# Kernel tuning notes

Hardware: AMD Instinct MI355X
Metric: run time of the kernel (lower is better)

## Reference

```python
import jax, jax.numpy as jnp
import numpy as np

N = 400000      # total atoms across batch of molecules
E = 1600000     # directed edges (avg degree 4)
G = 4096        # number of graphs (molecules)
F_IN = 78       # atomic feature size
H = 128         # gnn hidden dims (gnn_0 = gnn_1 = 128)
FF0, FF1 = 256, 128


def _lin(k, fan_in, fan_out):
    return jax.random.normal(k, (fan_in, fan_out), jnp.float32) / np.sqrt(fan_in).astype(np.float32)


def setup_inputs() -> dict:
    key = jax.random.key(0)
    ks = jax.random.split(key, 10)
    x = jax.random.normal(ks[0], (N, F_IN), jnp.float32)
    edge_index = jax.random.randint(ks[1], (2, E), 0, N, dtype=jnp.int64)
    # sorted graph ids, guaranteed non-empty segments (empty segment -> -inf under max pool)
    batch = (jnp.arange(N, dtype=jnp.int64) * G) // N
    return {
        'x': x, 'edge_index': edge_index, 'batch': batch,
        'W0': _lin(ks[2], F_IN, H), 'b0': jnp.zeros((H,), jnp.float32),
        'W1': _lin(ks[3], H, H),    'b1': jnp.zeros((H,), jnp.float32),
        'Wf0': _lin(ks[4], H, FF0), 'bf0': jnp.zeros((FF0,), jnp.float32),
        'Wf1': _lin(ks[5], FF0, FF1), 'bf1': jnp.zeros((FF1,), jnp.float32),
    }


def _gcn_conv(h, W, b, src, dst, dinv):
    # GCNConv with add_self_loops=True, symmetric normalization.
    hw = h @ W                                     # [N, out]
    norm = dinv[src] * dinv[dst]                   # [E]
    msg = hw[src] * norm[:, None]                  # gather + scale
    agg = jax.ops.segment_sum(msg, dst, num_segments=h.shape[0])
    agg = agg + hw * (dinv * dinv)[:, None]        # self-loop contribution
    return agg + b


def reference(x, edge_index, batch, W0, b0, W1, b1, Wf0, bf0, Wf1, bf1):
    src, dst = edge_index[0], edge_index[1]
    # degree of A + I computed at target nodes (PyG gcn_norm uses col)
    deg = jax.ops.segment_sum(jnp.ones((E,), x.dtype), dst, num_segments=N) + 1.0
    dinv = jax.lax.rsqrt(deg)

    h = jax.nn.relu(_gcn_conv(x, W0, b0, src, dst, dinv))
    h = jax.nn.relu(_gcn_conv(h, W1, b1, src, dst, dinv))

    g = jax.ops.segment_max(h, batch, num_segments=G)   # global max pool [G, H]

    g = jax.nn.relu(g @ Wf0 + bf0)   # dropout is identity in eval
    g = jax.nn.relu(g @ Wf1 + bf1)
    return g
```

## Files before the change

kernel.cpp:

```cpp
#include <hip/hip_runtime.h>
#include <cstdint>
#include <cstddef>

#define NATOMS 400000
#define NEDGES 1600000
#define NGRAPH 4096
#define F_INN  78
#define HDIM   128
#define FF0D   256
#define FF1D   128

typedef __attribute__((ext_vector_type(8))) short short8;
typedef __attribute__((ext_vector_type(4))) short short4v;
typedef __attribute__((ext_vector_type(4))) float f32x4;
typedef __attribute__((ext_vector_type(2))) float f32x2;

static __device__ __forceinline__ short f2bf(float f) {
    unsigned u = __builtin_bit_cast(unsigned, f);
    unsigned r = (u + 0x7fffu + ((u >> 16) & 1u)) >> 16;
    return (short)r;
}
static __device__ __forceinline__ float bf2f(unsigned short u) {
    return __builtin_bit_cast(float, ((unsigned)u) << 16);
}

__global__ __launch_bounds__(256) void k_degi(const int* __restrict__ dst,
                                              int* __restrict__ deg,
                                              int* __restrict__ rank, int E) {
    int e = blockIdx.x * 256 + threadIdx.x;
    if (e < E) rank[e] = atomicAdd(&deg[dst[e]], 1);
}

__global__ __launch_bounds__(256) void k_scan1(int* __restrict__ data,
                                               int* __restrict__ blockSums,
                                               float* __restrict__ dinv, int n) {
    __shared__ int ts[256];
    const int base = blockIdx.x * 1024 + threadIdx.x * 4;
    int v[4];
    #pragma unroll
    for (int j = 0; j < 4; ++j) v[j] = (base + j < n) ? data[base + j] : 0;
    #pragma unroll
    for (int j = 0; j < 4; ++j)
        if (base + j < n) dinv[base + j] = rsqrtf((float)v[j] + 1.0f);
    const int tot = v[0] + v[1] + v[2] + v[3];
    ts[threadIdx.x] = tot;
    __syncthreads();
    #pragma unroll
    for (int off = 1; off < 256; off <<= 1) {
        int t = (threadIdx.x >= off) ? ts[threadIdx.x - off] : 0;
        __syncthreads();
        ts[threadIdx.x] += t;
        __syncthreads();
    }
    int run = ts[threadIdx.x] - tot;
    #pragma unroll
    for (int j = 0; j < 4; ++j) {
        if (base + j < n) data[base + j] = run;
        run += v[j];
    }
    if (threadIdx.x == 255) blockSums[blockIdx.x] = ts[255];
}

__global__ __launch_bounds__(512) void k_scan2(int* __restrict__ blockSums, int nb) {
    __shared__ int ts[512];
    int v = (threadIdx.x < nb) ? blockSums[threadIdx.x] : 0;
    ts[threadIdx.x] = v;
    __syncthreads();
    #pragma unroll
    for (int off = 1; off < 512; off <<= 1) {
        int t = (threadIdx.x >= off) ? ts[threadIdx.x - off] : 0;
        __syncthreads();
        ts[threadIdx.x] += t;
        __syncthreads();
    }
    if (threadIdx.x < nb) blockSums[threadIdx.x] = ts[threadIdx.x] - v;
}

__global__ __launch_bounds__(256) void k_scan3(int* __restrict__ data,
                                               const int* __restrict__ blockSums,
                                               int n, int total) {
    const int off = blockSums[blockIdx.x];
    const int base = blockIdx.x * 1024 + threadIdx.x * 4;
    #pragma unroll
    for (int j = 0; j < 4; ++j)
        if (base + j < n) data[base + j] += off;
    if (blockIdx.x == 0 && threadIdx.x == 0) data[n] = total;
}

__global__ __launch_bounds__(256) void k_fill(const int* __restrict__ src,
                                              const int* __restrict__ dst,
                                              const int* __restrict__ row_start,
                                              const int* __restrict__ rank,
                                              int2* __restrict__ csr_ev,
                                              const float* __restrict__ dinv, int E) {
    int e = blockIdx.x * 256 + threadIdx.x;
    if (e >= E) return;
    int d = dst[e];
    int s = src[e];
    int pos = row_start[d] + rank[e];
    float norm = dinv[s] * dinv[d];
    csr_ev[pos] = make_int2(s, __builtin_bit_cast(int, norm));
}

template<int KC, int KSRC>
__global__ __launch_bounds__(64) void k_packw(const float* __restrict__ W,
                                              short* __restrict__ wf) {
    int t = blockIdx.x * 64 + threadIdx.x;
    int f = t >> 6, lane = t & 63;
    int ct = f / KC, kc = f % KC;
    int n  = ct * 16 + (lane & 15);
    int k0 = kc * 32 + (lane >> 4) * 8;
    short8 o;
    #pragma unroll
    for (int j = 0; j < 8; ++j) {
        int k = k0 + j;
        float v = (k < KSRC) ? W[(size_t)k * 128 + n] : 0.f;
        o[j] = f2bf(v);
    }
    *(short8*)(wf + (size_t)t * 8) = o;
}

template<int KC, bool F32IN, int KSRC>
__global__ __launch_bounds__(256) void k_gemm_mfma(
    const void* __restrict__ inv, const short* __restrict__ wfrag,
    short* __restrict__ outp, int M)
{
    constexpr int NFRAG = 8 * KC;
    __shared__ short lds_w[NFRAG * 64 * 8];

    const int tid = threadIdx.x;
    #pragma unroll
    for (int it = 0; it < NFRAG * 64 / 256; ++it) {
        int t = it * 256 + tid;
        *(short8*)(lds_w + (size_t)t * 8) = *(const short8*)(wfrag + (size_t)t * 8);
    }
    __syncthreads();

    const int lane = tid & 63;
    const int m = lane & 15, q = lane >> 4;
    const int gw = blockIdx.x * 4 + (tid >> 6);
    const int NW = gridDim.x * 4;
    const int NTILE = M / 16;

    auto load_afr = [&](int tile, short8* afr) {
        const int rowa = tile * 16 + m;
        if constexpr (F32IN) {
            const float* xr = (const float*)inv + (size_t)rowa * KSRC;
            #pragma unroll
            for (int kc = 0; kc < KC; ++kc) {
                const int k0 = kc * 32 + q * 8;
                float v[8];
                #pragma unroll
                for (int j = 0; j < 8; ++j) v[j] = 0.f;
                if (k0 < KSRC) {
                    #pragma unroll
                    for (int p = 0; p < 4; ++p) {
                        int k = k0 + 2 * p;
                        if (k < KSRC) {
                            f32x2 t = *(const f32x2*)(xr + k);
                            v[2 * p] = t.x; v[2 * p + 1] = t.y;
                        }
                    }
                }
                short8 a;
                #pragma unroll
                for (int j = 0; j < 8; ++j) a[j] = f2bf(v[j]);
                afr[kc] = a;
            }
        } else {
            const short* xr = (const short*)inv + (size_t)rowa * KSRC;
            #pragma unroll
            for (int kc = 0; kc < KC; ++kc)
                afr[kc] = *(const short8*)(xr + kc * 32 + q * 8);
        }
    };

    short8 afr[KC], afrN[KC];
    load_afr(gw, afr);

    for (int t = gw; t < NTILE; t += NW) {
        const int tn = t + NW;
        if (tn < NTILE) load_afr(tn, afrN);

        f32x4 acc[8];
        #pragma unroll
        for (int ct = 0; ct < 8; ++ct) acc[ct] = (f32x4){0.f, 0.f, 0.f, 0.f};
        #pragma unroll
        for (int kc = 0; kc < KC; ++kc)
            #pragma unroll
            for (int ct = 0; ct < 8; ++ct) {
                const short8 wv = *(const short8*)(lds_w + ((size_t)((ct * KC + kc) * 64 + lane)) * 8);
                acc[ct] = __builtin_amdgcn_mfma_f32_16x16x32_bf16(wv, afr[kc], acc[ct], 0, 0, 0);
            }

        const size_t nodeoff = (size_t)(t * 16 + m) * 128;
        #pragma unroll
        for (int ct = 0; ct < 8; ++ct) {
            short4v o;
            o.x = f2bf(acc[ct][0]);
            o.y = f2bf(acc[ct][1]);
            o.z = f2bf(acc[ct][2]);
            o.w = f2bf(acc[ct][3]);
            *(short4v*)(outp + nodeoff + ct * 16 + q * 4) = o;
        }

        #pragma unroll
        for (int kc = 0; kc < KC; ++kc) afr[kc] = afrN[kc];
    }
}

__global__ __launch_bounds__(256) void k_gather_bf(
    const unsigned short* __restrict__ hw, unsigned short* __restrict__ agg,
    const int* __restrict__ row_start, const int2* __restrict__ csr_ev,
    const float* __restrict__ dinv, const float* __restrict__ bias, int Nn)
{
    const int n  = blockIdx.x * 16 + (threadIdx.x >> 4);
    const int c8 = (threadIdx.x & 15) * 8;
    const float dv = dinv[n];
    const float d2 = dv * dv;

    float acc[8];
    {
        const short8 sv = *(const short8*)(hw + (size_t)n * HDIM + c8);
        #pragma unroll
        for (int j = 0; j < 8; ++j)
            acc[j] = fmaf(bf2f((unsigned short)sv[j]), d2, bias[c8 + j]);
    }

    const int s0 = row_start[n], s1 = row_start[n + 1];
    int i = s0;
    for (; i + 3 < s1; i += 4) {
        const int2 e0 = csr_ev[i];
        const int2 e1 = csr_ev[i + 1];
        const int2 e2 = csr_ev[i + 2];
        const int2 e3 = csr_ev[i + 3];
        const short8 r0 = *(const short8*)(hw + (size_t)e0.x * HDIM + c8);
        const short8 r1 = *(const short8*)(hw + (size_t)e1.x * HDIM + c8);
        const short8 r2 = *(const short8*)(hw + (size_t)e2.x * HDIM + c8);
        const short8 r3 = *(const short8*)(hw + (size_t)e3.x * HDIM + c8);
        const float w0 = __builtin_bit_cast(float, e0.y);
        const float w1 = __builtin_bit_cast(float, e1.y);
        const float w2 = __builtin_bit_cast(float, e2.y);
        const float w3 = __builtin_bit_cast(float, e3.y);
        #pragma unroll
        for (int j = 0; j < 8; ++j) acc[j] = fmaf(bf2f((unsigned short)r0[j]), w0, acc[j]);
        #pragma unroll
        for (int j = 0; j < 8; ++j) acc[j] = fmaf(bf2f((unsigned short)r1[j]), w1, acc[j]);
        #pragma unroll
        for (int j = 0; j < 8; ++j) acc[j] = fmaf(bf2f((unsigned short)r2[j]), w2, acc[j]);
        #pragma unroll
        for (int j = 0; j < 8; ++j) acc[j] = fmaf(bf2f((unsigned short)r3[j]), w3, acc[j]);
    }
    for (; i < s1; ++i) {
        const int2 e0 = csr_ev[i];
        const short8 r0 = *(const short8*)(hw + (size_t)e0.x * HDIM + c8);
        const float w0 = __builtin_bit_cast(float, e0.y);
        #pragma unroll
        for (int j = 0; j < 8; ++j) acc[j] = fmaf(bf2f((unsigned short)r0[j]), w0, acc[j]);
    }

    short8 o;
    #pragma unroll
    for (int j = 0; j < 8; ++j) o[j] = f2bf(fmaxf(acc[j], 0.f));
    __builtin_nontemporal_store(o, (short8*)(agg + (size_t)n * HDIM + c8));
}

__global__ __launch_bounds__(256) void k_pool(
    const unsigned short* __restrict__ agg,
    const int* __restrict__ batch, float* __restrict__ out, int Nn)
{
    __shared__ int se[2];
    __shared__ float red[256];
    int g = blockIdx.x;
    if (threadIdx.x < 2) {
        int target = g + (int)threadIdx.x;
        int lo = 0, hi = Nn;
        while (lo < hi) {
            int mid = (lo + hi) >> 1;
            if (batch[mid] < target) lo = mid + 1; else hi = mid;
        }
        se[threadIdx.x] = lo;
    }
    __syncthreads();
    const int start = se[0], end = se[1];
    const int c = threadIdx.x & 127;
    const int half = threadIdx.x >> 7;
    float m = 0.f;
    for (int i = start + half; i < end; i += 2)
        m = fmaxf(m, bf2f(__builtin_nontemporal_load(agg + (size_t)i * HDIM + c)));
    red[threadIdx.x] = m;
    __syncthreads();
    if (half == 0)
        out[(size_t)g * HDIM + c] = fmaxf(red[threadIdx.x], red[threadIdx.x + 128]);
}

template<int K, int NC, bool OUT_RELU_BIAS>
__global__ __launch_bounds__(256) void k_gemm(
    const float* __restrict__ in, const float* __restrict__ W,
    const float* __restrict__ out_bias, float* __restrict__ out0, int M)
{
    constexpr int BK = 32;
    constexpr int TC = NC / 8;
    constexpr int TR = 256 / TC;
    constexpr int ROWS = TR * 8;
    constexpr int XST = ROWS + 4;

    __shared__ float xs[BK][XST];
    __shared__ float ws[BK][NC];

    const int tid = threadIdx.x;
    const int tc  = tid % TC;
    const int tr  = tid / TC;
    const int row0 = blockIdx.x * ROWS;

    float acc[8][8];
    #pragma unroll
    for (int i = 0; i < 8; ++i)
        #pragma unroll
        for (int j = 0; j < 8; ++j) acc[i][j] = 0.f;

    for (int k0 = 0; k0 < K; k0 += BK) {
        {
            constexpr int TASKS = BK * NC / 4;
            #pragma unroll
            for (int it = 0; it < TASKS / 256; ++it) {
                int t  = it * 256 + tid;
                int wk = t / (NC / 4);
                int wc = (t % (NC / 4)) * 4;
                *(float4*)(&ws[wk][wc]) = *(const float4*)(W + (size_t)(k0 + wk) * NC + wc);
            }
        }
        {
            constexpr int TASKS = ROWS * BK / 4;
            #pragma unroll
            for (int it = 0; it < TASKS / 256; ++it) {
                int t   = it * 256 + tid;
                int r   = t / (BK / 4);
                int kq  = (t % (BK / 4)) * 4;
                float4 x4 = *(const float4*)(in + (size_t)(row0 + r) * K + k0 + kq);
                xs[kq + 0][r] = x4.x; xs[kq + 1][r] = x4.y;
                xs[kq + 2][r] = x4.z; xs[kq + 3][r] = x4.w;
            }
        }
        __syncthreads();
        #pragma unroll 8
        for (int kk = 0; kk < BK; ++kk) {
            float a[8], b[8];
            #pragma unroll
            for (int i = 0; i < 8; ++i) a[i] = xs[kk][tr * 8 + i];
            #pragma unroll
            for (int j = 0; j < 8; ++j) b[j] = ws[kk][tc * 8 + j];
            #pragma unroll
            for (int i = 0; i < 8; ++i)
                #pragma unroll
                for (int j = 0; j < 8; ++j)
                    acc[i][j] = fmaf(a[i], b[j], acc[i][j]);
        }
        __syncthreads();
    }

    #pragma unroll
    for (int i = 0; i < 8; ++i) {
        const int row = row0 + tr * 8 + i;
        #pragma unroll
        for (int jq = 0; jq < 2; ++jq) {
            const int col = tc * 8 + jq * 4;
            float4 v;
            v.x = acc[i][jq * 4 + 0]; v.y = acc[i][jq * 4 + 1];
            v.z = acc[i][jq * 4 + 2]; v.w = acc[i][jq * 4 + 3];
            if constexpr (OUT_RELU_BIAS) {
                const float4 bb = *(const float4*)(out_bias + col);
                v.x = fmaxf(v.x + bb.x, 0.f); v.y = fmaxf(v.y + bb.y, 0.f);
                v.z = fmaxf(v.z + bb.z, 0.f); v.w = fmaxf(v.w + bb.w, 0.f);
            }
            *(float4*)(out0 + (size_t)row * NC + col) = v;
        }
    }
}

extern "C" void kernel_launch(void* const* d_in, const int* in_sizes, int n_in,
                              void* d_out, int out_size, void* d_ws, size_t ws_size,
                              hipStream_t stream) {
    const float* x    = (const float*)d_in[0];
    const int*   ei   = (const int*)d_in[1];
    const int*   batch= (const int*)d_in[2];
    const float* W0   = (const float*)d_in[3];
    const float* b0   = (const float*)d_in[4];
    const float* W1   = (const float*)d_in[5];
    const float* b1   = (const float*)d_in[6];
    const float* Wf0  = (const float*)d_in[7];
    const float* bf0  = (const float*)d_in[8];
    const float* Wf1  = (const float*)d_in[9];
    const float* bf1  = (const float*)d_in[10];
    float* out = (float*)d_out;

    const int* srcI = ei;
    const int* dstI = ei + NEDGES;

    constexpr int SCAN_NBLK = (NATOMS + 1023) / 1024;

    char* base = (char*)d_ws;
    unsigned short* hwA  = (unsigned short*)(base + 0);
    unsigned short* aggB = (unsigned short*)(base + 102400000);
    int*   rank      = (int*)(base + 102400000);
    float* dinv      = (float*)(base + 204800000);
    int*   row_start = (int*)(base + 206400000);
    int2*  csr_ev    = (int2*)(base + 208000064);
    int*   blockSums = (int*)(base + 220800064);
    float* pool      = (float*)(base + 220802112);
    float* ff0       = (float*)(base + 222899264);
    short* wf0       = (short*)(base + 227093568);
    short* wf1       = (short*)(base + 227118144);

    hipMemsetAsync(row_start, 0, (size_t)(NATOMS + 1) * sizeof(int), stream);
    k_degi<<<(NEDGES + 255) / 256, 256, 0, stream>>>(dstI, row_start, rank, NEDGES);
    k_scan1<<<SCAN_NBLK, 256, 0, stream>>>(row_start, blockSums, dinv, NATOMS);
    k_scan2<<<1, 512, 0, stream>>>(blockSums, SCAN_NBLK);
    k_scan3<<<SCAN_NBLK, 256, 0, stream>>>(row_start, blockSums, NATOMS, NEDGES);
    k_fill<<<(NEDGES + 255) / 256, 256, 0, stream>>>(srcI, dstI, row_start, rank,
                                                     csr_ev, dinv, NEDGES);

    k_packw<3, F_INN><<<8 * 3, 64, 0, stream>>>(W0, wf0);
    k_packw<4, HDIM><<<8 * 4, 64, 0, stream>>>(W1, wf1);

    k_gemm_mfma<3, true, F_INN><<<1024, 256, 0, stream>>>(x, wf0, (short*)hwA, NATOMS);
    k_gather_bf<<<NATOMS / 16, 256, 0, stream>>>(hwA, aggB, row_start, csr_ev,
                                                 dinv, b0, NATOMS);

    k_gemm_mfma<4, false, HDIM><<<1024, 256, 0, stream>>>(aggB, wf1, (short*)hwA, NATOMS);
    k_gather_bf<<<NATOMS / 16, 256, 0, stream>>>(hwA, aggB, row_start, csr_ev,
                                                 dinv, b1, NATOMS);

    k_pool<<<NGRAPH, 256, 0, stream>>>(aggB, batch, pool, NATOMS);

    k_gemm<HDIM, FF0D, true><<<NGRAPH / 64, 256, 0, stream>>>(pool, Wf0, bf0, ff0, NGRAPH);
    k_gemm<FF0D, FF1D, true><<<NGRAPH / 128, 256, 0, stream>>>(ff0, Wf1, bf1, out, NGRAPH);
}
```

Measured before the change: 718.4 us.

## Split gathers into column halves and fuse max-pool into second gather

Each edge-gather now runs as two launches that each handle 64 of the 128 feature columns, so the random-access working set per pass is half the hw table and should fit better in cache. The second layer's gather also computes the global max pool in place: it reduces each block's values per graph with wave shuffles and shared memory, then applies atomicMax on the float bits into a zeroed pool buffer. This removes the separate pool kernel and the write and re-read of the layer-2 output. In exchange it reads the CSR arrays twice, adds atomics, and assumes each 32-node block spans at most two graphs and that pooled values are non-negative.

```diff
diff --git a/kernel.cpp b/kernel.cpp
--- a/kernel.cpp
+++ b/kernel.cpp
@@ -209,13 +209,15 @@
     }
 }
 
-__global__ __launch_bounds__(256) void k_gather_bf(
+template<bool POOL>
+__global__ __launch_bounds__(256) void k_gather_half(
     const unsigned short* __restrict__ hw, unsigned short* __restrict__ agg,
     const int* __restrict__ row_start, const int2* __restrict__ csr_ev,
-    const float* __restrict__ dinv, const float* __restrict__ bias, int Nn)
+    const float* __restrict__ dinv, const float* __restrict__ bias,
+    const int* __restrict__ batch, int* __restrict__ pool, int half)
 {
-    const int n  = blockIdx.x * 16 + (threadIdx.x >> 4);
-    const int c8 = (threadIdx.x & 15) * 8;
+    const int n  = blockIdx.x * 32 + (threadIdx.x >> 3);
+    const int c8 = half * 64 + (threadIdx.x & 7) * 8;
     const float dv = dinv[n];
     const float d2 = dv * dv;
 
@@ -259,39 +261,53 @@
         for (int j = 0; j < 8; ++j) acc[j] = fmaf(bf2f((unsigned short)r0[j]), w0, acc[j]);
     }
 
-    short8 o;
-    #pragma unroll
-    for (int j = 0; j < 8; ++j) o[j] = f2bf(fmaxf(acc[j], 0.f));
-    __builtin_nontemporal_store(o, (short8*)(agg + (size_t)n * HDIM + c8));
-}
-
-__global__ __launch_bounds__(256) void k_pool(
-    const unsigned short* __restrict__ agg,
-    const int* __restrict__ batch, float* __restrict__ out, int Nn)
-{
-    __shared__ int se[2];
-    __shared__ float red[256];
-    int g = blockIdx.x;
-    if (threadIdx.x < 2) {
-        int target = g + (int)threadIdx.x;
-        int lo = 0, hi = Nn;
-        while (lo < hi) {
-            int mid = (lo + hi) >> 1;
-            if (batch[mid] < target) lo = mid + 1; else hi = mid;
-        }
-        se[threadIdx.x] = lo;
-    }
-    __syncthreads();
-    const int start = se[0], end = se[1];
-    const int c = threadIdx.x & 127;
-    const int half = threadIdx.x >> 7;
-    float m = 0.f;
-    for (int i = start + half; i < end; i += 2)
-        m = fmaxf(m, bf2f(__builtin_nontemporal_load(agg + (size_t)i * HDIM + c)));
-    red[threadIdx.x] = m;
-    __syncthreads();
-    if (half == 0)
-        out[(size_t)g * HDIM + c] = fmaxf(red[threadIdx.x], red[threadIdx.x + 128]);
+    if constexpr (!POOL) {
+        short8 o;
+        #pragma unroll
+        for (int j = 0; j < 8; ++j) o[j] = f2bf(fmaxf(acc[j], 0.f));
+        __builtin_nontemporal_store(o, (short8*)(agg + (size_t)n * HDIM + c8));
+    } else {
+        const int gbase = batch[blockIdx.x * 32];
+        const int glast = batch[blockIdx.x * 32 + 31];
+        const int idx   = batch[n] - gbase;
+
+        float red[2][8];
+        #pragma unroll
+        for (int s = 0; s < 2; ++s)
+            #pragma unroll
+            for (int j = 0; j < 8; ++j)
+                red[s][j] = (idx == s) ? fmaxf(acc[j], 0.f) : 0.f;
+
+        #pragma unroll
+        for (int msk = 8; msk <= 32; msk <<= 1)
+            #pragma unroll
+            for (int s = 0; s < 2; ++s)
+                #pragma unroll
+                for (int j = 0; j < 8; ++j)
+                    red[s][j] = fmaxf(red[s][j], __shfl_xor(red[s][j], msk));
+
+        __shared__ float sm[4][2][64];
+        const int wid  = threadIdx.x >> 6;
+        const int lane = threadIdx.x & 63;
+        if (lane < 8) {
+            #pragma unroll
+            for (int s = 0; s < 2; ++s)
+                #pragma unroll
+                for (int j = 0; j < 8; ++j)
+                    sm[wid][s][lane * 8 + j] = red[s][j];
+        }
+        __syncthreads();
+        if (threadIdx.x < 128) {
+            const int s = threadIdx.x >> 6;
+            const int f = threadIdx.x & 63;
+            if (s == 0 || glast != gbase) {
+                float m = fmaxf(fmaxf(sm[0][s][f], sm[1][s][f]),
+                                fmaxf(sm[2][s][f], sm[3][s][f]));
+                atomicMax(pool + (size_t)(gbase + s) * HDIM + half * 64 + f,
+                          __builtin_bit_cast(int, m));
+            }
+        }
+    }
 }
 
 template<int K, int NC, bool OUT_RELU_BIAS>
@@ -413,6 +429,7 @@
     short* wf1       = (short*)(base + 227118144);
 
     hipMemsetAsync(row_start, 0, (size_t)(NATOMS + 1) * sizeof(int), stream);
+    hipMemsetAsync(pool, 0, (size_t)NGRAPH * HDIM * sizeof(float), stream);
     k_degi<<<(NEDGES + 255) / 256, 256, 0, stream>>>(dstI, row_start, rank, NEDGES);
     k_scan1<<<SCAN_NBLK, 256, 0, stream>>>(row_start, blockSums, dinv, NATOMS);
     k_scan2<<<1, 512, 0, stream>>>(blockSums, SCAN_NBLK);
@@ -424,14 +441,16 @@
     k_packw<4, HDIM><<<8 * 4, 64, 0, stream>>>(W1, wf1);
 
     k_gemm_mfma<3, true, F_INN><<<1024, 256, 0, stream>>>(x, wf0, (short*)hwA, NATOMS);
-    k_gather_bf<<<NATOMS / 16, 256, 0, stream>>>(hwA, aggB, row_start, csr_ev,
-                                                 dinv, b0, NATOMS);
+    k_gather_half<false><<<NATOMS / 32, 256, 0, stream>>>(hwA, aggB, row_start, csr_ev,
+                                                          dinv, b0, nullptr, nullptr, 0);
+    k_gather_half<false><<<NATOMS / 32, 256, 0, stream>>>(hwA, aggB, row_start, csr_ev,
+                                                          dinv, b0, nullptr, nullptr, 1);
 
     k_gemm_mfma<4, false, HDIM><<<1024, 256, 0, stream>>>(aggB, wf1, (short*)hwA, NATOMS);
-    k_gather_bf<<<NATOMS / 16, 256, 0, stream>>>(hwA, aggB, row_start, csr_ev,
-                                                 dinv, b1, NATOMS);
-
-    k_pool<<<NGRAPH, 256, 0, stream>>>(aggB, batch, pool, NATOMS);
+    k_gather_half<true><<<NATOMS / 32, 256, 0, stream>>>(hwA, nullptr, row_start, csr_ev,
+                                                         dinv, b1, batch, (int*)pool, 0);
+    k_gather_half<true><<<NATOMS / 32, 256, 0, stream>>>(hwA, nullptr, row_start, csr_ev,
+                                                         dinv, b1, batch, (int*)pool, 1);
 
     k_gemm<HDIM, FF0D, true><<<NGRAPH / 64, 256, 0, stream>>>(pool, Wf0, bf0, ff0, NGRAPH);
     k_gemm<FF0D, FF1D, true><<<NGRAPH / 128, 256, 0, stream>>>(ff0, Wf1, bf1, out, NGRAPH);
```

Measured after the change: 677.9 us. 1.06x faster.
